# Optimization experiments

Measured on AMD Instinct MI355X. Metric: run time of the kernel, lower is better.

Reference implementation:

```python
import jax, jax.numpy as jnp
import numpy as np
from functools import partial

T_DEC, B, T_ENC = 32, 64, 128
SENT, EMB, DEC, ATT, VOC = 4096, 300, 512, 512, 32000


def setup_inputs() -> dict:
    key = jax.random.key(0)
    ks = jax.random.split(key, 24)
    w = lambda k, s: jax.random.normal(k, s, jnp.float32) * 0.02
    d = lambda k, s: jax.random.normal(k, s, jnp.float32)
    z = lambda n: jnp.zeros((n,), jnp.float32)
    return {
        'expl': d(ks[0], (T_DEC, B, EMB)),
        'enc_out_s1': d(ks[1], (T_ENC, B, SENT)),
        'enc_out_s2': d(ks[2], (T_ENC, B, SENT)),
        's1_embed': d(ks[3], (B, SENT)),
        's2_embed': d(ks[4], (B, SENT)),
        'W_ctx': w(ks[5], (DEC, 4 * SENT)), 'b_ctx': z(DEC),
        'Wq1': w(ks[6], (ATT, DEC)), 'bq1': z(ATT),
        'Wk1': w(ks[7], (ATT, SENT)), 'bk1': z(ATT),
        'Wv1': w(ks[8], (ATT, SENT)), 'bv1': z(ATT),
        'Wq2': w(ks[9], (ATT, DEC)), 'bq2': z(ATT),
        'Wk2': w(ks[10], (ATT, SENT)), 'bk2': z(ATT),
        'Wv2': w(ks[11], (ATT, SENT)), 'bv2': z(ATT),
        'W_in': w(ks[12], (DEC, 2 * ATT + EMB)), 'b_in': z(DEC),
        'W_ih': w(ks[13], (3 * DEC, DEC)), 'b_ih': z(3 * DEC),
        'W_hh': w(ks[14], (3 * DEC, DEC)), 'b_hh': z(3 * DEC),
        'W_voc': w(ks[15], (VOC, DEC)), 'b_voc': z(VOC),
    }


def _forward(expl, enc_out_s1, enc_out_s2, s1_embed, s2_embed,
             W_ctx, b_ctx, Wq1, bq1, Wk1, bk1, Wv1, bv1,
             Wq2, bq2, Wk2, bk2, Wv2, bv2,
             W_in, b_in, W_ih, b_ih, W_hh, b_hh, W_voc, b_voc):
    # context feature: [B, 4*SENT]
    ctx_feat = jnp.concatenate(
        [s1_embed, s2_embed, jnp.abs(s1_embed - s2_embed), s1_embed * s2_embed], axis=1)
    # init hidden == context (both come from context_proj with use_init=True)
    h0 = ctx_feat @ W_ctx.T + b_ctx  # [B, DEC]

    # encoder projections are loop-invariant (same value every timestep in the
    # original Python loop), so compute once: keys/values [T_ENC, B, ATT]
    keys1 = jnp.tanh(enc_out_s1 @ Wk1.T + bk1)
    vals1 = jnp.tanh(enc_out_s1 @ Wv1.T + bv1)
    keys2 = jnp.tanh(enc_out_s2 @ Wk2.T + bk2)
    vals2 = jnp.tanh(enc_out_s2 @ Wv2.T + bv2)

    def step(h, x_t):
        # dual dot-product attention using previous hidden state as query
        q1 = jnp.tanh(h @ Wq1.T + bq1)                    # [B, ATT]
        a1 = jax.nn.softmax(jnp.einsum('bh,tbh->bt', q1, keys1), axis=-1)
        att1 = jnp.einsum('bt,tbh->bh', a1, vals1)        # [B, ATT]
        q2 = jnp.tanh(h @ Wq2.T + bq2)
        a2 = jax.nn.softmax(jnp.einsum('bh,tbh->bt', q2, keys2), axis=-1)
        att2 = jnp.einsum('bt,tbh->bh', a2, vals2)
        # project decoder input (dropout p=0 -> identity)
        x = jnp.concatenate([x_t, att1, att2], axis=1) @ W_in.T + b_in  # [B, DEC]
        # GRU cell (PyTorch convention)
        gi = x @ W_ih.T + b_ih
        gh = h @ W_hh.T + b_hh
        i_r, i_z, i_n = jnp.split(gi, 3, axis=1)
        h_r, h_z, h_n = jnp.split(gh, 3, axis=1)
        r = jax.nn.sigmoid(i_r + h_r)
        zg = jax.nn.sigmoid(i_z + h_z)
        n = jnp.tanh(i_n + r * h_n)
        h_new = (1.0 - zg) * n + zg * h
        return h_new, h_new

    _, outs = jax.lax.scan(step, h0, expl)   # outs: [T_DEC, B, DEC]
    return outs @ W_voc.T + b_voc            # [T_DEC, B, VOC]


def reference(expl, enc_out_s1, enc_out_s2, s1_embed, s2_embed,
              W_ctx, b_ctx, Wq1, bq1, Wk1, bk1, Wv1, bv1,
              Wq2, bq2, Wk2, bk2, Wv2, bv2,
              W_in, b_in, W_ih, b_ih, W_hh, b_hh, W_voc, b_voc):
    return _forward(expl, enc_out_s1, enc_out_s2, s1_embed, s2_embed,
                    W_ctx, b_ctx, Wq1, bq1, Wk1, bk1, Wv1, bv1,
                    Wq2, bq2, Wk2, bk2, Wv2, bv2,
                    W_in, b_in, W_ih, b_ih, W_hh, b_hh, W_voc, b_voc)
```

## Files before the change

### kernel.cpp

```cpp
#include <hip/hip_runtime.h>


typedef float    f32x4 __attribute__((ext_vector_type(4)));
typedef __bf16   bf16x8 __attribute__((ext_vector_type(8)));
typedef unsigned short u16x8 __attribute__((ext_vector_type(8)));

#define DEV __device__ __forceinline__

DEV unsigned short f2bf(float f) {
  unsigned u = __builtin_bit_cast(unsigned, f);
  u += 0x7fffu + ((u >> 16) & 1u);
  return (unsigned short)(u >> 16);
}
DEV float bf2f(unsigned short h) {
  return __builtin_bit_cast(float, (unsigned)h << 16);
}
DEV bf16x8 as_bf(u16x8 v) { return __builtin_bit_cast(bf16x8, v); }
DEV u16x8 zero8() {
  u16x8 r = {0, 0, 0, 0, 0, 0, 0, 0};
  return r;
}
DEV u16x8 pack8(float4 a, float4 b) {
  u16x8 r;
  r[0]=f2bf(a.x); r[1]=f2bf(a.y); r[2]=f2bf(a.z); r[3]=f2bf(a.w);
  r[4]=f2bf(b.x); r[5]=f2bf(b.y); r[6]=f2bf(b.z); r[7]=f2bf(b.w);
  return r;
}
DEV void gload16(const void* g, void* l) {
  __builtin_amdgcn_global_load_lds(
      (const __attribute__((address_space(1))) void*)g,
      (__attribute__((address_space(3))) void*)l, 16, 0, 0);
}
DEV float gru1(float ir, float iz, float inn, float hr, float hz, float hn,
               float ho) {
  float r = 1.f / (1.f + expf(-(ir + hr)));
  float z = 1.f / (1.f + expf(-(iz + hz)));
  float n = tanhf(inn + r * hn);
  return (1.f - z) * n + z * ho;
}

__global__ __launch_bounds__(256) void k_cvt(const float* __restrict__ s,
                                             unsigned short* __restrict__ d, int n) {
  int i = (blockIdx.x * 256 + threadIdx.x) * 4;
  if (i + 4 <= n) {
    float4 v = *(const float4*)(s + i);
    d[i] = f2bf(v.x); d[i+1] = f2bf(v.y); d[i+2] = f2bf(v.z); d[i+3] = f2bf(v.w);
  } else {
    for (; i < n; i++) d[i] = f2bf(s[i]);
  }
}

__global__ __launch_bounds__(256) void k_build_ctx(const float* __restrict__ s1,
                                                   const float* __restrict__ s2,
                                                   unsigned short* __restrict__ ctx) {
  int j = blockIdx.x * 256 + threadIdx.x;
  int b = j >> 14, jj = j & 16383;
  int f = jj >> 12, k = jj & 4095;
  float a = s1[b * 4096 + k], c = s2[b * 4096 + k];
  float v = (f == 0) ? a : (f == 1) ? c : (f == 2) ? fabsf(a - c) : a * c;
  ctx[j] = f2bf(v);
}

template<int EPI>
__global__ __launch_bounds__(256) void k_gemm_lds(
    const unsigned short* __restrict__ A, int lda,
    const unsigned short* __restrict__ B, int ldb, int K,
    unsigned short* __restrict__ obf0, unsigned short* __restrict__ obf1,
    float* __restrict__ of, int ofld,
    const float* __restrict__ bias0, const float* __restrict__ bias1)
{
  __shared__ __align__(16) unsigned short As[128 * 32];
  __shared__ __align__(16) unsigned short Bs[128 * 32];
  const int tid = threadIdx.x;
  const int r0 = blockIdx.x * 128, c0 = blockIdx.y * 128;
  const int lane = tid & 63, w = tid >> 6;
  const int wr = w >> 1, wc = w & 1;
  const int fr = lane & 15, fq = lane >> 4;
  f32x4 acc[4][4] = {};

  const int srow = tid >> 2, scol = (tid & 3) * 8;
  const unsigned short* gA0 = A + (size_t)(r0 + srow) * lda + scol;
  const unsigned short* gA1 = A + (size_t)(r0 + 64 + srow) * lda + scol;
  const unsigned short* gB0 = B + (size_t)(c0 + srow) * ldb + scol;
  const unsigned short* gB1 = B + (size_t)(c0 + 64 + srow) * ldb + scol;
  unsigned short* lA0 = As + tid * 8;
  unsigned short* lA1 = As + 2048 + tid * 8;
  unsigned short* lB0 = Bs + tid * 8;
  unsigned short* lB1 = Bs + 2048 + tid * 8;

  for (int k = 0; k < K; k += 32) {
    gload16(gA0 + k, lA0);
    gload16(gA1 + k, lA1);
    gload16(gB0 + k, lB0);
    gload16(gB1 + k, lB1);
    __syncthreads();

    u16x8 af[4], bfv[4];
    #pragma unroll
    for (int mi = 0; mi < 4; mi++)
      af[mi] = *(const u16x8*)&As[(wr * 64 + mi * 16 + fr) * 32 + fq * 8];
    #pragma unroll
    for (int nj = 0; nj < 4; nj++)
      bfv[nj] = *(const u16x8*)&Bs[(wc * 64 + nj * 16 + fr) * 32 + fq * 8];
    #pragma unroll
    for (int mi = 0; mi < 4; mi++)
      #pragma unroll
      for (int nj = 0; nj < 4; nj++)
        acc[mi][nj] = __builtin_amdgcn_mfma_f32_16x16x32_bf16(
            as_bf(af[mi]), as_bf(bfv[nj]), acc[mi][nj], 0, 0, 0);
    __syncthreads();
  }

  #pragma unroll
  for (int mi = 0; mi < 4; mi++)
  #pragma unroll
  for (int nj = 0; nj < 4; nj++) {
    f32x4 a = acc[mi][nj];
    #pragma unroll
    for (int j = 0; j < 4; j++) {
      int grow = r0 + wr * 64 + mi * 16 + fq * 4 + j;
      int gcol = c0 + wc * 64 + nj * 16 + fr;
      float v = a[j];
      if constexpr (EPI == 0) {
        float bias = gcol < 512 ? bias0[gcol] : bias1[gcol - 512];
        unsigned short r = f2bf(tanhf(v + bias));
        int prow = ((grow & 63) << 7) | (grow >> 6);
        (gcol < 512 ? obf0 : obf1)[(size_t)prow * 512 + (gcol & 511)] = r;
      } else {
        of[(size_t)grow * ofld + gcol] = v + bias0[gcol];
      }
    }
  }
}

template<int A_BF16, int B_BF16, int EPI>
__global__ __launch_bounds__(256) void k_gemm128(
    const void* __restrict__ Ap, int lda, const void* __restrict__ Bp, int ldb,
    int M, int N, int kper,
    unsigned short* __restrict__ obf0, unsigned short* __restrict__ obf1,
    float* __restrict__ of, const float* __restrict__ bias0,
    const float* __restrict__ bias1)
{
  __shared__ __align__(16) unsigned short As[128 * 32];
  __shared__ __align__(16) unsigned short Bs[128 * 32];
  const int tid = threadIdx.x;
  const int c0 = blockIdx.x * 128, r0 = blockIdx.y * 128;
  const int k0 = blockIdx.z * kper;
  if (EPI == 2) of += (size_t)blockIdx.z * M * N;

  const int lane = tid & 63, w = tid >> 6;
  const int wr = w >> 1, wc = w & 1;
  const int fr = lane & 15, fq = lane >> 4;

  f32x4 acc[4][4] = {};

  const int srow = tid >> 1, shalf = (tid & 1) * 16;

  for (int k = k0; k < k0 + kper; k += 32) {
    u16x8 a0, a1, b0, b1;
    {
      int gr = r0 + srow;
      if (gr < M) {
        if (A_BF16) {
          const unsigned short* a = (const unsigned short*)Ap + (size_t)gr * lda + k + shalf;
          a0 = *(const u16x8*)a; a1 = *(const u16x8*)(a + 8);
        } else {
          const float* a = (const float*)Ap + (size_t)gr * lda + k + shalf;
          float4 f0 = ((const float4*)a)[0], f1 = ((const float4*)a)[1];
          float4 f2 = ((const float4*)a)[2], f3 = ((const float4*)a)[3];
          a0 = pack8(f0, f1); a1 = pack8(f2, f3);
        }
      } else { a0 = zero8(); a1 = zero8(); }
    }
    {
      int gr = c0 + srow;
      if (B_BF16) {
        const unsigned short* p = (const unsigned short*)Bp + (size_t)gr * ldb + k + shalf;
        b0 = *(const u16x8*)p; b1 = *(const u16x8*)(p + 8);
      } else {
        const float* p = (const float*)Bp + (size_t)gr * ldb + k + shalf;
        float4 f0 = ((const float4*)p)[0], f1 = ((const float4*)p)[1];
        float4 f2 = ((const float4*)p)[2], f3 = ((const float4*)p)[3];
        b0 = pack8(f0, f1); b1 = pack8(f2, f3);
      }
    }
    *(u16x8*)&As[srow * 32 + shalf]     = a0;
    *(u16x8*)&As[srow * 32 + shalf + 8] = a1;
    *(u16x8*)&Bs[srow * 32 + shalf]     = b0;
    *(u16x8*)&Bs[srow * 32 + shalf + 8] = b1;
    __syncthreads();

    u16x8 af[4], bfv[4];
    #pragma unroll
    for (int mi = 0; mi < 4; mi++)
      af[mi] = *(const u16x8*)&As[(wr * 64 + mi * 16 + fr) * 32 + fq * 8];
    #pragma unroll
    for (int nj = 0; nj < 4; nj++)
      bfv[nj] = *(const u16x8*)&Bs[(wc * 64 + nj * 16 + fr) * 32 + fq * 8];
    #pragma unroll
    for (int mi = 0; mi < 4; mi++)
      #pragma unroll
      for (int nj = 0; nj < 4; nj++)
        acc[mi][nj] = __builtin_amdgcn_mfma_f32_16x16x32_bf16(
            as_bf(af[mi]), as_bf(bfv[nj]), acc[mi][nj], 0, 0, 0);
    __syncthreads();
  }

  #pragma unroll
  for (int mi = 0; mi < 4; mi++)
  #pragma unroll
  for (int nj = 0; nj < 4; nj++) {
    f32x4 a = acc[mi][nj];
    #pragma unroll
    for (int j = 0; j < 4; j++) {
      int grow = r0 + wr * 64 + mi * 16 + fq * 4 + j;
      int gcol = c0 + wc * 64 + nj * 16 + fr;
      if (grow < M) {
        float v = a[j];
        if constexpr (EPI == 1) {
          of[(size_t)grow * N + gcol] = v + bias0[gcol];
        } else if constexpr (EPI == 2) {
          of[(size_t)grow * N + gcol] = v;
        }
      }
    }
  }
}

__global__ __launch_bounds__(256) void k_reduce_h0(const float* __restrict__ part,
                                                   const float* __restrict__ b_ctx,
                                                   float* __restrict__ h,
                                                   unsigned short* __restrict__ h_bf) {
  int j = blockIdx.x * 256 + threadIdx.x;
  float s = b_ctx[j & 511];
  for (int z = 0; z < 8; z++) s += part[z * 32768 + j];
  h[j] = s;
  h_bf[j] = f2bf(s);
}

__global__ __launch_bounds__(256) void k_wf(const float* __restrict__ W_ih,
                                            const float* __restrict__ W_in,
                                            unsigned short* __restrict__ wf_att,
                                            float* __restrict__ wfx) {
  __shared__ float wl[8][512];
  int ic = blockIdx.x, jc = blockIdx.y, tid = threadIdx.x;
  for (int x = tid; x < 8 * 512; x += 256)
    wl[x >> 9][x & 511] = W_ih[(ic * 8 + (x >> 9)) * 512 + (x & 511)];
  __syncthreads();
  int j = jc * 256 + tid;
  if (j >= 1324) return;
  float acc[8] = {};
  for (int d = 0; d < 512; d++) {
    float win = W_in[d * 1324 + j];
    #pragma unroll
    for (int r = 0; r < 8; r++) acc[r] += wl[r][d] * win;
  }
  for (int r = 0; r < 8; r++) {
    int i = ic * 8 + r;
    if (j < 300) wfx[i * 300 + j] = acc[r];
    else         wf_att[i * 1024 + (j - 300)] = f2bf(acc[r]);
  }
}

__global__ __launch_bounds__(256) void k_bfull(const float* __restrict__ W_ih,
                                               const float* __restrict__ b_in,
                                               const float* __restrict__ b_ih,
                                               float* __restrict__ bfull) {
  int i = blockIdx.x * 256 + threadIdx.x;
  if (i >= 1536) return;
  float acc = b_ih[i];
  for (int d = 0; d < 512; d++) acc += W_ih[i * 512 + d] * b_in[d];
  bfull[i] = acc;
}

__global__ __launch_bounds__(256) void k_gix(const float* __restrict__ expl,
                                             const float* __restrict__ wfx,
                                             float* __restrict__ gi_x) {
  __shared__ float el[16][300];
  int rc = blockIdx.x, ic = blockIdx.y, tid = threadIdx.x;
  for (int x = tid; x < 16 * 300; x += 256)
    el[x / 300][x % 300] = expl[(size_t)(rc * 16 + x / 300) * 300 + (x % 300)];
  __syncthreads();
  int c = ic * 256 + tid;
  float acc[16] = {};
  for (int k = 0; k < 300; k++) {
    float wv = wfx[c * 300 + k];
    #pragma unroll
    for (int r = 0; r < 16; r++) acc[r] += el[r][k] * wv;
  }
  for (int r = 0; r < 16; r++) gi_x[(size_t)(rc * 16 + r) * 1536 + c] = acc[r];
}

__global__ __launch_bounds__(256) void k_mv64f(
    const unsigned short* __restrict__ A,
    const unsigned short* __restrict__ B,
    const float* __restrict__ bq1, const float* __restrict__ bq2,
    const float* __restrict__ b_hh,
    float* __restrict__ qf, float* __restrict__ ghf)
{
  __shared__ __align__(16) unsigned short AL[16 * 2048];
  __shared__ __align__(16) unsigned short BL[16 * 2048];
  const int tid = threadIdx.x;
  const int n0 = blockIdx.x * 64;
  const int srow = tid >> 2, scol = (tid & 3) * 8;

  #pragma unroll
  for (int c = 0; c < 16; c++) {
    gload16(A + (size_t)srow * 512 + c * 32 + scol, AL + c * 2048 + tid * 8);
    gload16(B + (size_t)(n0 + srow) * 512 + c * 32 + scol, BL + c * 2048 + tid * 8);
  }
  __syncthreads();

  const int lane = tid & 63, w = tid >> 6;
  const int fr = lane & 15, fq = lane >> 4;
  f32x4 acc[4] = {};
  #pragma unroll
  for (int c = 0; c < 16; c++) {
    u16x8 af = *(const u16x8*)(AL + c * 2048 + (w * 16 + fr) * 32 + fq * 8);
    #pragma unroll
    for (int nj = 0; nj < 4; nj++) {
      u16x8 bv = *(const u16x8*)(BL + c * 2048 + (nj * 16 + fr) * 32 + fq * 8);
      acc[nj] = __builtin_amdgcn_mfma_f32_16x16x32_bf16(as_bf(af), as_bf(bv), acc[nj], 0, 0, 0);
    }
  }
  #pragma unroll
  for (int nj = 0; nj < 4; nj++) {
    #pragma unroll
    for (int j = 0; j < 4; j++) {
      int row = w * 16 + fq * 4 + j;
      int col = n0 + nj * 16 + fr;
      float v = acc[nj][j];
      if (col < 512)       qf[(size_t)row * 1024 + col] = tanhf(v + bq1[col]);
      else if (col < 1024) qf[(size_t)row * 1024 + col] = tanhf(v + bq2[col - 512]);
      else                 ghf[(size_t)row * 1536 + (col - 1024)] = v + b_hh[col - 1024];
    }
  }
}

__global__ __launch_bounds__(256) void k_att(
    const float* __restrict__ qf,
    const unsigned short* __restrict__ keys1, const unsigned short* __restrict__ keys2,
    const unsigned short* __restrict__ vals1, const unsigned short* __restrict__ vals2,
    unsigned short* __restrict__ att_bf)
{
  const int id = blockIdx.x, side = id >> 6, b = id & 63;
  const int tid = threadIdx.x;
  __shared__ float qv[512];
  __shared__ float sred[128][2];
  __shared__ float pr[128];

  for (int i = tid; i < 512; i += 256)
    qv[i] = qf[(size_t)b * 1024 + side * 512 + i];
  __syncthreads();

  const unsigned short* keys = side ? keys2 : keys1;
  {
    int tt = tid >> 1, half = tid & 1;
    const u16x8* krow = (const u16x8*)(keys + ((size_t)(b * 128 + tt)) * 512 + half * 256);
    float acc = 0.f;
    #pragma unroll 4
    for (int k8 = 0; k8 < 32; k8++) {
      u16x8 kv = krow[k8];
      #pragma unroll
      for (int jj = 0; jj < 8; jj++) acc += qv[half * 256 + k8 * 8 + jj] * bf2f(kv[jj]);
    }
    sred[tt][half] = acc;
  }
  __syncthreads();

  if (tid < 64) {
    float s0 = sred[tid][0] + sred[tid][1];
    float s1 = sred[tid + 64][0] + sred[tid + 64][1];
    float m = fmaxf(s0, s1);
    #pragma unroll
    for (int off = 32; off; off >>= 1) m = fmaxf(m, __shfl_xor(m, off));
    float e0 = __expf(s0 - m), e1 = __expf(s1 - m);
    float ss = e0 + e1;
    #pragma unroll
    for (int off = 32; off; off >>= 1) ss += __shfl_xor(ss, off);
    float inv = 1.f / ss;
    pr[tid] = e0 * inv;
    pr[tid + 64] = e1 * inv;
  }
  __syncthreads();

  const unsigned short* vals = side ? vals2 : vals1;
  {
    int a0 = tid * 2;
    float acc0 = 0.f, acc1 = 0.f;
    for (int tt = 0; tt < 128; tt++) {
      float p = pr[tt];
      unsigned v = *(const unsigned*)(vals + ((size_t)(b * 128 + tt)) * 512 + a0);
      acc0 += p * bf2f((unsigned short)(v & 0xffffu));
      acc1 += p * bf2f((unsigned short)(v >> 16));
    }
    att_bf[(size_t)b * 1024 + side * 512 + a0]     = f2bf(acc0);
    att_bf[(size_t)b * 1024 + side * 512 + a0 + 1] = f2bf(acc1);
  }
}

__global__ __launch_bounds__(256) void k_giK(
    const unsigned short* __restrict__ att_bf,
    const unsigned short* __restrict__ wf_att,
    float* __restrict__ gip)
{
  __shared__ __align__(16) unsigned short AL[16 * 2048];
  __shared__ __align__(16) unsigned short BL[16 * 2048];
  const int tid = threadIdx.x;
  const int j = blockIdx.x % 24, kh = blockIdx.x / 24;
  const int n0 = j * 64, k0 = kh * 512;
  const int srow = tid >> 2, scol = (tid & 3) * 8;

  #pragma unroll
  for (int c = 0; c < 16; c++) {
    gload16(att_bf + (size_t)srow * 1024 + k0 + c * 32 + scol, AL + c * 2048 + tid * 8);
    gload16(wf_att + (size_t)(n0 + srow) * 1024 + k0 + c * 32 + scol, BL + c * 2048 + tid * 8);
  }
  __syncthreads();

  const int lane = tid & 63, w = tid >> 6;
  const int fr = lane & 15, fq = lane >> 4;
  f32x4 acc[4] = {};
  #pragma unroll
  for (int c = 0; c < 16; c++) {
    u16x8 af = *(const u16x8*)(AL + c * 2048 + (w * 16 + fr) * 32 + fq * 8);
    #pragma unroll
    for (int nj = 0; nj < 4; nj++) {
      u16x8 bv = *(const u16x8*)(BL + c * 2048 + (nj * 16 + fr) * 32 + fq * 8);
      acc[nj] = __builtin_amdgcn_mfma_f32_16x16x32_bf16(as_bf(af), as_bf(bv), acc[nj], 0, 0, 0);
    }
  }
  #pragma unroll
  for (int nj = 0; nj < 4; nj++) {
    #pragma unroll
    for (int jj = 0; jj < 4; jj++) {
      int row = w * 16 + fq * 4 + jj;
      int col = n0 + nj * 16 + fr;
      gip[(size_t)(kh * 64 + row) * 1536 + col] = acc[nj][jj];
    }
  }
}

__global__ __launch_bounds__(512) void k_gru2(
    int t, const float* __restrict__ gip, const float* __restrict__ gi_x,
    const float* __restrict__ bfull, const float* __restrict__ ghf,
    float* __restrict__ hst, unsigned short* __restrict__ h_bf,
    unsigned short* __restrict__ outs_bf)
{
  const int b = blockIdx.x, d = threadIdx.x;
  size_t gb = (size_t)(t * 64 + b) * 1536;
  float ir = gip[(size_t)b * 1536 + d] + gip[(size_t)(64 + b) * 1536 + d]
           + gi_x[gb + d] + bfull[d];
  float iz = gip[(size_t)b * 1536 + 512 + d] + gip[(size_t)(64 + b) * 1536 + 512 + d]
           + gi_x[gb + 512 + d] + bfull[512 + d];
  float inn = gip[(size_t)b * 1536 + 1024 + d] + gip[(size_t)(64 + b) * 1536 + 1024 + d]
           + gi_x[gb + 1024 + d] + bfull[1024 + d];
  float hv = gru1(ir, iz, inn,
                  ghf[b * 1536 + d], ghf[b * 1536 + 512 + d], ghf[b * 1536 + 1024 + d],
                  hst[b * 512 + d]);
  hst[b * 512 + d] = hv;
  unsigned short bf = f2bf(hv);
  h_bf[b * 512 + d] = bf;
  outs_bf[(size_t)(t * 64 + b) * 512 + d] = bf;
}

extern "C" void kernel_launch(void* const* d_in, const int* in_sizes, int n_in,
                              void* d_out, int out_size, void* d_ws, size_t ws_size,
                              hipStream_t stream) {
  const float* expl  = (const float*)d_in[0];
  const float* enc1  = (const float*)d_in[1];
  const float* enc2  = (const float*)d_in[2];
  const float* s1e   = (const float*)d_in[3];
  const float* s2e   = (const float*)d_in[4];
  const float* W_ctx = (const float*)d_in[5];
  const float* b_ctx = (const float*)d_in[6];
  const float* Wq1   = (const float*)d_in[7];
  const float* bq1   = (const float*)d_in[8];
  const float* Wk1   = (const float*)d_in[9];
  const float* bk1   = (const float*)d_in[10];
  const float* Wv1   = (const float*)d_in[11];
  const float* bv1   = (const float*)d_in[12];
  const float* Wq2   = (const float*)d_in[13];
  const float* bq2   = (const float*)d_in[14];
  const float* Wk2   = (const float*)d_in[15];
  const float* bk2   = (const float*)d_in[16];
  const float* Wv2   = (const float*)d_in[17];
  const float* bv2   = (const float*)d_in[18];
  const float* W_in  = (const float*)d_in[19];
  const float* b_in  = (const float*)d_in[20];
  const float* W_ih  = (const float*)d_in[21];
  const float* b_ih  = (const float*)d_in[22];
  const float* W_hh  = (const float*)d_in[23];
  const float* b_hh  = (const float*)d_in[24];
  const float* W_voc = (const float*)d_in[25];
  const float* b_voc = (const float*)d_in[26];
  float* out = (float*)d_out;

  char* ws = (char*)d_ws;
  unsigned short* keys1  = (unsigned short*)(ws + 0);
  unsigned short* vals1  = (unsigned short*)(ws + 8388608);
  unsigned short* keys2  = (unsigned short*)(ws + 16777216);
  unsigned short* vals2  = (unsigned short*)(ws + 25165824);
  unsigned short* encbf  = (unsigned short*)(ws + 33554432);
  unsigned short* wkv    = (unsigned short*)(ws + 100663296);
  unsigned short* wvoc   = (unsigned short*)(ws + 109051904);
  unsigned short* wcat   = (unsigned short*)(ws + 141819904);
  unsigned short* wf_att = (unsigned short*)(ws + 144441344);
  float*          wfx    = (float*)(ws + 147587072);
  float*          bfull  = (float*)(ws + 149430272);
  float*          gi_x   = (float*)(ws + 149436416);
  unsigned short* ctx_bf = (unsigned short*)(ws + 162019328);
  float*          part   = (float*)(ws + 164116480);
  float*          hst    = (float*)(ws + 165165056);
  unsigned short* h_bf   = (unsigned short*)(ws + 165296128);
  float*          qf     = (float*)(ws + 165361664);
  float*          ghf    = (float*)(ws + 165623808);
  unsigned short* att_bf = (unsigned short*)(ws + 166410240);
  unsigned short* outs_bf= (unsigned short*)(ws + 166541312);
  float*          gip    = (float*)(ws + 168638464);

  auto cvt = [&](const float* s, unsigned short* d, int n) {
    k_cvt<<<(n + 1023) / 1024, 256, 0, stream>>>(s, d, n);
  };

  cvt(enc1, encbf, 8192 * 4096);
  cvt(Wk1, wkv, 512 * 4096);
  cvt(Wv1, wkv + 512 * 4096, 512 * 4096);
  k_gemm_lds<0><<<dim3(64, 8), 256, 0, stream>>>(
      encbf, 4096, wkv, 4096, 4096, keys1, vals1, nullptr, 0, bk1, bv1);
  cvt(enc2, encbf, 8192 * 4096);
  cvt(Wk2, wkv, 512 * 4096);
  cvt(Wv2, wkv + 512 * 4096, 512 * 4096);
  k_gemm_lds<0><<<dim3(64, 8), 256, 0, stream>>>(
      encbf, 4096, wkv, 4096, 4096, keys2, vals2, nullptr, 0, bk2, bv2);

  cvt(W_voc, wvoc, 32000 * 512);
  cvt(Wq1, wcat, 512 * 512);
  cvt(Wq2, wcat + 512 * 512, 512 * 512);
  cvt(W_hh, wcat + 1024 * 512, 1536 * 512);

  k_wf<<<dim3(192, 6), 256, 0, stream>>>(W_ih, W_in, wf_att, wfx);
  k_bfull<<<6, 256, 0, stream>>>(W_ih, b_in, b_ih, bfull);
  k_gix<<<dim3(128, 6), 256, 0, stream>>>(expl, wfx, gi_x);

  k_build_ctx<<<4096, 256, 0, stream>>>(s1e, s2e, ctx_bf);
  k_gemm128<1, 0, 2><<<dim3(4, 1, 8), 256, 0, stream>>>(
      ctx_bf, 16384, W_ctx, 16384, 64, 512, 2048,
      nullptr, nullptr, part, nullptr, nullptr);
  k_reduce_h0<<<128, 256, 0, stream>>>(part, b_ctx, hst, h_bf);

  for (int t = 0; t < 32; t++) {
    k_mv64f<<<40, 256, 0, stream>>>(h_bf, wcat, bq1, bq2, b_hh, qf, ghf);
    k_att<<<128, 256, 0, stream>>>(qf, keys1, keys2, vals1, vals2, att_bf);
    k_giK<<<48, 256, 0, stream>>>(att_bf, wf_att, gip);
    k_gru2<<<64, 512, 0, stream>>>(t, gip, gi_x, bfull, ghf, hst, h_bf, outs_bf);
  }

  k_gemm_lds<1><<<dim3(16, 250), 256, 0, stream>>>(
      outs_bf, 512, wvoc, 512, 512, nullptr, nullptr, out, 32000, b_voc, nullptr);
}
```

Before: 1.635 ms.

## Batch fp32-to-bf16 conversions, merge K/V GEMMs, remap vocab GEMM blocks for XCD locality

Replaces the ten separate conversion launches with one segmented conversion kernel that looks up each element's segment from a cumulative-size table. The two encoder K/V projection GEMMs become one launch over both sides, and each side gets its own bf16 buffer, which enlarges the workspace. The vocabulary projection GEMM uses a 1D grid whose block index is remapped so that each XCD handles a contiguous range of column tiles, aiming at better L2 reuse of W_voc. The intent is to cut launch count and serialization and to improve cache locality; the costs are a per-thread segment search and more workspace memory.

```diff
diff --git a/kernel.cpp b/kernel.cpp
--- a/kernel.cpp
+++ b/kernel.cpp
@@ -16,16 +16,6 @@
   return __builtin_bit_cast(float, (unsigned)h << 16);
 }
 DEV bf16x8 as_bf(u16x8 v) { return __builtin_bit_cast(bf16x8, v); }
-DEV u16x8 zero8() {
-  u16x8 r = {0, 0, 0, 0, 0, 0, 0, 0};
-  return r;
-}
-DEV u16x8 pack8(float4 a, float4 b) {
-  u16x8 r;
-  r[0]=f2bf(a.x); r[1]=f2bf(a.y); r[2]=f2bf(a.z); r[3]=f2bf(a.w);
-  r[4]=f2bf(b.x); r[5]=f2bf(b.y); r[6]=f2bf(b.z); r[7]=f2bf(b.w);
-  return r;
-}
 DEV void gload16(const void* g, void* l) {
   __builtin_amdgcn_global_load_lds(
       (const __attribute__((address_space(1))) void*)g,
@@ -39,15 +29,22 @@
   return (1.f - z) * n + z * ho;
 }
 
-__global__ __launch_bounds__(256) void k_cvt(const float* __restrict__ s,
-                                             unsigned short* __restrict__ d, int n) {
-  int i = (blockIdx.x * 256 + threadIdx.x) * 4;
-  if (i + 4 <= n) {
-    float4 v = *(const float4*)(s + i);
-    d[i] = f2bf(v.x); d[i+1] = f2bf(v.y); d[i+2] = f2bf(v.z); d[i+3] = f2bf(v.w);
-  } else {
-    for (; i < n; i++) d[i] = f2bf(s[i]);
-  }
+#define NSEG 10
+struct CvtSegs {
+  const float* src[NSEG];
+  unsigned short* dst[NSEG];
+  int cum4[NSEG + 1];
+};
+
+__global__ __launch_bounds__(256) void k_cvt_multi(CvtSegs segs, int total4) {
+  int i4 = blockIdx.x * 256 + threadIdx.x;
+  if (i4 >= total4) return;
+  int s = 0;
+  while (i4 >= segs.cum4[s + 1]) s++;
+  int off = (i4 - segs.cum4[s]) * 4;
+  float4 v = *(const float4*)(segs.src[s] + off);
+  unsigned short* d = segs.dst[s] + off;
+  d[0] = f2bf(v.x); d[1] = f2bf(v.y); d[2] = f2bf(v.z); d[3] = f2bf(v.w);
 }
 
 __global__ __launch_bounds__(256) void k_build_ctx(const float* __restrict__ s1,
@@ -61,34 +58,42 @@
   ctx[j] = f2bf(v);
 }
 
-template<int EPI>
-__global__ __launch_bounds__(256) void k_gemm_lds(
-    const unsigned short* __restrict__ A, int lda,
-    const unsigned short* __restrict__ B, int ldb, int K,
-    unsigned short* __restrict__ obf0, unsigned short* __restrict__ obf1,
-    float* __restrict__ of, int ofld,
-    const float* __restrict__ bias0, const float* __restrict__ bias1)
+__global__ __launch_bounds__(256) void k_gemm_kv(
+    const unsigned short* __restrict__ enc1bf, const unsigned short* __restrict__ enc2bf,
+    const unsigned short* __restrict__ wkv1, const unsigned short* __restrict__ wkv2,
+    unsigned short* __restrict__ keys1, unsigned short* __restrict__ vals1,
+    unsigned short* __restrict__ keys2, unsigned short* __restrict__ vals2,
+    const float* __restrict__ bk1, const float* __restrict__ bv1,
+    const float* __restrict__ bk2, const float* __restrict__ bv2)
 {
   __shared__ __align__(16) unsigned short As[128 * 32];
   __shared__ __align__(16) unsigned short Bs[128 * 32];
   const int tid = threadIdx.x;
-  const int r0 = blockIdx.x * 128, c0 = blockIdx.y * 128;
+  const int side = blockIdx.x >> 6;
+  const int r0 = (blockIdx.x & 63) * 128, c0 = blockIdx.y * 128;
+  const unsigned short* A = side ? enc2bf : enc1bf;
+  const unsigned short* B = side ? wkv2 : wkv1;
+  unsigned short* kout = side ? keys2 : keys1;
+  unsigned short* vout = side ? vals2 : vals1;
+  const float* bk = side ? bk2 : bk1;
+  const float* bv = side ? bv2 : bv1;
+
   const int lane = tid & 63, w = tid >> 6;
   const int wr = w >> 1, wc = w & 1;
   const int fr = lane & 15, fq = lane >> 4;
   f32x4 acc[4][4] = {};
 
   const int srow = tid >> 2, scol = (tid & 3) * 8;
-  const unsigned short* gA0 = A + (size_t)(r0 + srow) * lda + scol;
-  const unsigned short* gA1 = A + (size_t)(r0 + 64 + srow) * lda + scol;
-  const unsigned short* gB0 = B + (size_t)(c0 + srow) * ldb + scol;
-  const unsigned short* gB1 = B + (size_t)(c0 + 64 + srow) * ldb + scol;
+  const unsigned short* gA0 = A + (size_t)(r0 + srow) * 4096 + scol;
+  const unsigned short* gA1 = A + (size_t)(r0 + 64 + srow) * 4096 + scol;
+  const unsigned short* gB0 = B + (size_t)(c0 + srow) * 4096 + scol;
+  const unsigned short* gB1 = B + (size_t)(c0 + 64 + srow) * 4096 + scol;
   unsigned short* lA0 = As + tid * 8;
   unsigned short* lA1 = As + 2048 + tid * 8;
   unsigned short* lB0 = Bs + tid * 8;
   unsigned short* lB1 = Bs + 2048 + tid * 8;
 
-  for (int k = 0; k < K; k += 32) {
+  for (int k = 0; k < 4096; k += 32) {
     gload16(gA0 + k, lA0);
     gload16(gA1 + k, lA1);
     gload16(gB0 + k, lB0);
@@ -120,40 +125,95 @@
     for (int j = 0; j < 4; j++) {
       int grow = r0 + wr * 64 + mi * 16 + fq * 4 + j;
       int gcol = c0 + wc * 64 + nj * 16 + fr;
-      float v = a[j];
-      if constexpr (EPI == 0) {
-        float bias = gcol < 512 ? bias0[gcol] : bias1[gcol - 512];
-        unsigned short r = f2bf(tanhf(v + bias));
-        int prow = ((grow & 63) << 7) | (grow >> 6);
-        (gcol < 512 ? obf0 : obf1)[(size_t)prow * 512 + (gcol & 511)] = r;
-      } else {
-        of[(size_t)grow * ofld + gcol] = v + bias0[gcol];
-      }
-    }
-  }
-}
-
-template<int A_BF16, int B_BF16, int EPI>
-__global__ __launch_bounds__(256) void k_gemm128(
-    const void* __restrict__ Ap, int lda, const void* __restrict__ Bp, int ldb,
-    int M, int N, int kper,
-    unsigned short* __restrict__ obf0, unsigned short* __restrict__ obf1,
-    float* __restrict__ of, const float* __restrict__ bias0,
-    const float* __restrict__ bias1)
+      float bias = gcol < 512 ? bk[gcol] : bv[gcol - 512];
+      unsigned short r = f2bf(tanhf(a[j] + bias));
+      int prow = ((grow & 63) << 7) | (grow >> 6);
+      (gcol < 512 ? kout : vout)[(size_t)prow * 512 + (gcol & 511)] = r;
+    }
+  }
+}
+
+__global__ __launch_bounds__(256) void k_gemm_voc(
+    const unsigned short* __restrict__ A,
+    const unsigned short* __restrict__ B,
+    float* __restrict__ of, const float* __restrict__ bias)
+{
+  const int L = blockIdx.x;
+  const int xcd = L & 7, k = L >> 3;
+  const int rb = k & 15, cb = xcd * 32 + (k >> 4);
+  if (cb >= 250) return;
+  const int r0 = rb * 128, c0 = cb * 128;
+
+  __shared__ __align__(16) unsigned short As[128 * 32];
+  __shared__ __align__(16) unsigned short Bs[128 * 32];
+  const int tid = threadIdx.x;
+  const int lane = tid & 63, w = tid >> 6;
+  const int wr = w >> 1, wc = w & 1;
+  const int fr = lane & 15, fq = lane >> 4;
+  f32x4 acc[4][4] = {};
+
+  const int srow = tid >> 2, scol = (tid & 3) * 8;
+  const unsigned short* gA0 = A + (size_t)(r0 + srow) * 512 + scol;
+  const unsigned short* gA1 = A + (size_t)(r0 + 64 + srow) * 512 + scol;
+  const unsigned short* gB0 = B + (size_t)(c0 + srow) * 512 + scol;
+  const unsigned short* gB1 = B + (size_t)(c0 + 64 + srow) * 512 + scol;
+  unsigned short* lA0 = As + tid * 8;
+  unsigned short* lA1 = As + 2048 + tid * 8;
+  unsigned short* lB0 = Bs + tid * 8;
+  unsigned short* lB1 = Bs + 2048 + tid * 8;
+
+  for (int kk = 0; kk < 512; kk += 32) {
+    gload16(gA0 + kk, lA0);
+    gload16(gA1 + kk, lA1);
+    gload16(gB0 + kk, lB0);
+    gload16(gB1 + kk, lB1);
+    __syncthreads();
+
+    u16x8 af[4], bfv[4];
+    #pragma unroll
+    for (int mi = 0; mi < 4; mi++)
+      af[mi] = *(const u16x8*)&As[(wr * 64 + mi * 16 + fr) * 32 + fq * 8];
+    #pragma unroll
+    for (int nj = 0; nj < 4; nj++)
+      bfv[nj] = *(const u16x8*)&Bs[(wc * 64 + nj * 16 + fr) * 32 + fq * 8];
+    #pragma unroll
+    for (int mi = 0; mi < 4; mi++)
+      #pragma unroll
+      for (int nj = 0; nj < 4; nj++)
+        acc[mi][nj] = __builtin_amdgcn_mfma_f32_16x16x32_bf16(
+            as_bf(af[mi]), as_bf(bfv[nj]), acc[mi][nj], 0, 0, 0);
+    __syncthreads();
+  }
+
+  #pragma unroll
+  for (int mi = 0; mi < 4; mi++)
+  #pragma unroll
+  for (int nj = 0; nj < 4; nj++) {
+    f32x4 a = acc[mi][nj];
+    #pragma unroll
+    for (int j = 0; j < 4; j++) {
+      int grow = r0 + wr * 64 + mi * 16 + fq * 4 + j;
+      int gcol = c0 + wc * 64 + nj * 16 + fr;
+      of[(size_t)grow * 32000 + gcol] = a[j] + bias[gcol];
+    }
+  }
+}
+
+__global__ __launch_bounds__(256) void k_gemm_h0(
+    const unsigned short* __restrict__ Ap, int lda, const float* __restrict__ Bp,
+    int ldb, int M, int N, int kper, float* __restrict__ of)
 {
   __shared__ __align__(16) unsigned short As[128 * 32];
   __shared__ __align__(16) unsigned short Bs[128 * 32];
   const int tid = threadIdx.x;
   const int c0 = blockIdx.x * 128, r0 = blockIdx.y * 128;
   const int k0 = blockIdx.z * kper;
-  if (EPI == 2) of += (size_t)blockIdx.z * M * N;
+  of += (size_t)blockIdx.z * M * N;
 
   const int lane = tid & 63, w = tid >> 6;
   const int wr = w >> 1, wc = w & 1;
   const int fr = lane & 15, fq = lane >> 4;
-
   f32x4 acc[4][4] = {};
-
   const int srow = tid >> 1, shalf = (tid & 1) * 16;
 
   for (int k = k0; k < k0 + kper; k += 32) {
@@ -161,28 +221,21 @@
     {
       int gr = r0 + srow;
       if (gr < M) {
-        if (A_BF16) {
-          const unsigned short* a = (const unsigned short*)Ap + (size_t)gr * lda + k + shalf;
-          a0 = *(const u16x8*)a; a1 = *(const u16x8*)(a + 8);
-        } else {
-          const float* a = (const float*)Ap + (size_t)gr * lda + k + shalf;
-          float4 f0 = ((const float4*)a)[0], f1 = ((const float4*)a)[1];
-          float4 f2 = ((const float4*)a)[2], f3 = ((const float4*)a)[3];
-          a0 = pack8(f0, f1); a1 = pack8(f2, f3);
-        }
-      } else { a0 = zero8(); a1 = zero8(); }
+        const unsigned short* a = Ap + (size_t)gr * lda + k + shalf;
+        a0 = *(const u16x8*)a; a1 = *(const u16x8*)(a + 8);
+      } else {
+        u16x8 z = {0,0,0,0,0,0,0,0}; a0 = z; a1 = z;
+      }
     }
     {
       int gr = c0 + srow;
-      if (B_BF16) {
-        const unsigned short* p = (const unsigned short*)Bp + (size_t)gr * ldb + k + shalf;
-        b0 = *(const u16x8*)p; b1 = *(const u16x8*)(p + 8);
-      } else {
-        const float* p = (const float*)Bp + (size_t)gr * ldb + k + shalf;
-        float4 f0 = ((const float4*)p)[0], f1 = ((const float4*)p)[1];
-        float4 f2 = ((const float4*)p)[2], f3 = ((const float4*)p)[3];
-        b0 = pack8(f0, f1); b1 = pack8(f2, f3);
-      }
+      const float* p = Bp + (size_t)gr * ldb + k + shalf;
+      float4 f0 = ((const float4*)p)[0], f1 = ((const float4*)p)[1];
+      float4 f2 = ((const float4*)p)[2], f3 = ((const float4*)p)[3];
+      b0[0]=f2bf(f0.x); b0[1]=f2bf(f0.y); b0[2]=f2bf(f0.z); b0[3]=f2bf(f0.w);
+      b0[4]=f2bf(f1.x); b0[5]=f2bf(f1.y); b0[6]=f2bf(f1.z); b0[7]=f2bf(f1.w);
+      b1[0]=f2bf(f2.x); b1[1]=f2bf(f2.y); b1[2]=f2bf(f2.z); b1[3]=f2bf(f2.w);
+      b1[4]=f2bf(f3.x); b1[5]=f2bf(f3.y); b1[6]=f2bf(f3.z); b1[7]=f2bf(f3.w);
     }
     *(u16x8*)&As[srow * 32 + shalf]     = a0;
     *(u16x8*)&As[srow * 32 + shalf + 8] = a1;
@@ -215,14 +268,7 @@
     for (int j = 0; j < 4; j++) {
       int grow = r0 + wr * 64 + mi * 16 + fq * 4 + j;
       int gcol = c0 + wc * 64 + nj * 16 + fr;
-      if (grow < M) {
-        float v = a[j];
-        if constexpr (EPI == 1) {
-          of[(size_t)grow * N + gcol] = v + bias0[gcol];
-        } else if constexpr (EPI == 2) {
-          of[(size_t)grow * N + gcol] = v;
-        }
-      }
+      if (grow < M) of[(size_t)grow * N + gcol] = a[j];
     }
   }
 }
@@ -501,52 +547,55 @@
   unsigned short* vals1  = (unsigned short*)(ws + 8388608);
   unsigned short* keys2  = (unsigned short*)(ws + 16777216);
   unsigned short* vals2  = (unsigned short*)(ws + 25165824);
-  unsigned short* encbf  = (unsigned short*)(ws + 33554432);
-  unsigned short* wkv    = (unsigned short*)(ws + 100663296);
-  unsigned short* wvoc   = (unsigned short*)(ws + 109051904);
-  unsigned short* wcat   = (unsigned short*)(ws + 141819904);
-  unsigned short* wf_att = (unsigned short*)(ws + 144441344);
-  float*          wfx    = (float*)(ws + 147587072);
-  float*          bfull  = (float*)(ws + 149430272);
-  float*          gi_x   = (float*)(ws + 149436416);
-  unsigned short* ctx_bf = (unsigned short*)(ws + 162019328);
-  float*          part   = (float*)(ws + 164116480);
-  float*          hst    = (float*)(ws + 165165056);
-  unsigned short* h_bf   = (unsigned short*)(ws + 165296128);
-  float*          qf     = (float*)(ws + 165361664);
-  float*          ghf    = (float*)(ws + 165623808);
-  unsigned short* att_bf = (unsigned short*)(ws + 166410240);
-  unsigned short* outs_bf= (unsigned short*)(ws + 166541312);
-  float*          gip    = (float*)(ws + 168638464);
-
-  auto cvt = [&](const float* s, unsigned short* d, int n) {
-    k_cvt<<<(n + 1023) / 1024, 256, 0, stream>>>(s, d, n);
-  };
-
-  cvt(enc1, encbf, 8192 * 4096);
-  cvt(Wk1, wkv, 512 * 4096);
-  cvt(Wv1, wkv + 512 * 4096, 512 * 4096);
-  k_gemm_lds<0><<<dim3(64, 8), 256, 0, stream>>>(
-      encbf, 4096, wkv, 4096, 4096, keys1, vals1, nullptr, 0, bk1, bv1);
-  cvt(enc2, encbf, 8192 * 4096);
-  cvt(Wk2, wkv, 512 * 4096);
-  cvt(Wv2, wkv + 512 * 4096, 512 * 4096);
-  k_gemm_lds<0><<<dim3(64, 8), 256, 0, stream>>>(
-      encbf, 4096, wkv, 4096, 4096, keys2, vals2, nullptr, 0, bk2, bv2);
-
-  cvt(W_voc, wvoc, 32000 * 512);
-  cvt(Wq1, wcat, 512 * 512);
-  cvt(Wq2, wcat + 512 * 512, 512 * 512);
-  cvt(W_hh, wcat + 1024 * 512, 1536 * 512);
+  unsigned short* encbf1 = (unsigned short*)(ws + 33554432);
+  unsigned short* encbf2 = (unsigned short*)(ws + 100663296);
+  unsigned short* wkv1   = (unsigned short*)(ws + 167772160);
+  unsigned short* wkv2   = (unsigned short*)(ws + 176160768);
+  unsigned short* wvoc   = (unsigned short*)(ws + 184549376);
+  unsigned short* wcat   = (unsigned short*)(ws + 217317376);
+  unsigned short* wf_att = (unsigned short*)(ws + 219938816);
+  float*          wfx    = (float*)(ws + 223084544);
+  float*          bfull  = (float*)(ws + 224927744);
+  float*          gi_x   = (float*)(ws + 224933888);
+  unsigned short* ctx_bf = (unsigned short*)(ws + 237516800);
+  float*          part   = (float*)(ws + 239613952);
+  float*          hst    = (float*)(ws + 240662528);
+  unsigned short* h_bf   = (unsigned short*)(ws + 240793600);
+  float*          qf     = (float*)(ws + 240859136);
+  float*          ghf    = (float*)(ws + 241121280);
+  unsigned short* att_bf = (unsigned short*)(ws + 241514496);
+  unsigned short* outs_bf= (unsigned short*)(ws + 241645568);
+  float*          gip    = (float*)(ws + 243742720);
+
+  {
+    CvtSegs segs;
+    const float* srcs[NSEG] = { enc1, enc2, Wk1, Wv1, Wk2, Wv2, W_voc,
+                                Wq1, Wq2, W_hh };
+    unsigned short* dsts[NSEG] = { encbf1, encbf2, wkv1, wkv1 + 512*4096,
+                                   wkv2, wkv2 + 512*4096, wvoc,
+                                   wcat, wcat + 512*512, wcat + 1024*512 };
+    int ns[NSEG] = { 8192*4096, 8192*4096, 512*4096, 512*4096, 512*4096,
+                     512*4096, 32000*512, 512*512, 512*512, 1536*512 };
+    int cum = 0;
+    for (int s = 0; s < NSEG; s++) {
+      segs.src[s] = srcs[s]; segs.dst[s] = dsts[s];
+      segs.cum4[s] = cum; cum += ns[s] / 4;
+    }
+    segs.cum4[NSEG] = cum;
+    k_cvt_multi<<<(cum + 255) / 256, 256, 0, stream>>>(segs, cum);
+  }
+
+  k_gemm_kv<<<dim3(128, 8), 256, 0, stream>>>(
+      encbf1, encbf2, wkv1, wkv2, keys1, vals1, keys2, vals2,
+      bk1, bv1, bk2, bv2);
 
   k_wf<<<dim3(192, 6), 256, 0, stream>>>(W_ih, W_in, wf_att, wfx);
   k_bfull<<<6, 256, 0, stream>>>(W_ih, b_in, b_ih, bfull);
   k_gix<<<dim3(128, 6), 256, 0, stream>>>(expl, wfx, gi_x);
 
   k_build_ctx<<<4096, 256, 0, stream>>>(s1e, s2e, ctx_bf);
-  k_gemm128<1, 0, 2><<<dim3(4, 1, 8), 256, 0, stream>>>(
-      ctx_bf, 16384, W_ctx, 16384, 64, 512, 2048,
-      nullptr, nullptr, part, nullptr, nullptr);
+  k_gemm_h0<<<dim3(4, 1, 8), 256, 0, stream>>>(
+      ctx_bf, 16384, W_ctx, 16384, 64, 512, 2048, part);
   k_reduce_h0<<<128, 256, 0, stream>>>(part, b_ctx, hst, h_bf);
 
   for (int t = 0; t < 32; t++) {
@@ -556,6 +605,5 @@
     k_gru2<<<64, 512, 0, stream>>>(t, gip, gi_x, bfull, ghf, hst, h_bf, outs_bf);
   }
 
-  k_gemm_lds<1><<<dim3(16, 250), 256, 0, stream>>>(
-      outs_bf, 512, wvoc, 512, 512, nullptr, nullptr, out, 32000, b_voc, nullptr);
-}
+  k_gemm_voc<<<4096, 256, 0, stream>>>(outs_bf, wvoc, out, b_voc);
+}
```

Result: no change. 1.628 ms (-0.4%).
